# Performance work log

Hardware: AMD Instinct MI355X
Metric: run time of the kernel (lower is better)

Reference implementation:

```python
import jax, jax.numpy as jnp
import numpy as np

N = 50000      # nodes
E = 800000     # edges (avg degree 16)
H = 128        # hidden_nf
NORM_FACTOR = 100.0   # normalization_factor, aggregation 'sum'
NORM_CONST = 1.0      # norm_constant (effective_constant = max(1, 1.0))
EPS = 1e-8


def silu(v):
    return v * jax.nn.sigmoid(v)


def setup_inputs() -> dict:
    key = jax.random.key(0)
    ks = jax.random.split(key, 16)
    IN_E = 2 * H + 2  # edge MLP input: h[row] | h[col] | [radial, edge_attr]

    def w(k, shape, scale=0.05):
        return jax.random.normal(k, shape, dtype=jnp.float32) * scale

    return {
        "h": jax.random.normal(ks[0], (N, H), dtype=jnp.float32),
        "x": jax.random.normal(ks[1], (N, 3), dtype=jnp.float32),
        "edge_index": jax.random.randint(ks[2], (2, E), 0, N, dtype=jnp.int32),
        "edge_attr": jax.random.normal(ks[3], (E, 1), dtype=jnp.float32),
        "node_mask": jnp.ones((N, 1), dtype=jnp.float32),
        "edge_mask": jnp.ones((E, 1), dtype=jnp.float32),
        # 2 stacked GCL layers (identical shapes -> stacked on leading dim)
        "gcl_e_w1": w(ks[4], (2, IN_E, H)), "gcl_e_b1": jnp.zeros((2, H), jnp.float32),
        "gcl_e_w2": w(ks[5], (2, H, H)),    "gcl_e_b2": jnp.zeros((2, H), jnp.float32),
        "gcl_a_w":  w(ks[6], (2, H, 1)),    "gcl_a_b":  jnp.zeros((2, 1), jnp.float32),
        "gcl_n_w1": w(ks[7], (2, 2 * H, H)),"gcl_n_b1": jnp.zeros((2, H), jnp.float32),
        "gcl_n_w2": w(ks[8], (2, H, H)),    "gcl_n_b2": jnp.zeros((2, H), jnp.float32),
        # EquivariantUpdate coord MLP (last layer xavier gain 0.001 -> tiny, no bias)
        "c_w1": w(ks[9], (IN_E, H)), "c_b1": jnp.zeros((H,), jnp.float32),
        "c_w2": w(ks[10], (H, H)),   "c_b2": jnp.zeros((H,), jnp.float32),
        "c_w3": w(ks[11], (H, 1), 0.001),
    }


def reference(h, x, edge_index, edge_attr, node_mask, edge_mask,
              gcl_e_w1, gcl_e_b1, gcl_e_w2, gcl_e_b2, gcl_a_w, gcl_a_b,
              gcl_n_w1, gcl_n_b1, gcl_n_w2, gcl_n_b2,
              c_w1, c_b1, c_w2, c_b2, c_w3):
    row, col = edge_index[0], edge_index[1]
    n_nodes = h.shape[0]

    # coord2diff
    diff = x[row] - x[col]                                  # [E,3]
    radial = jnp.sum(diff * diff, axis=1, keepdims=True)    # [E,1]
    norm = jnp.sqrt(radial + EPS)
    coord_diff = diff / (norm + NORM_CONST)

    # edge_attr = cat([distances, edge_attr])  -> edge_feat_nf = 2
    ea = jnp.concatenate([radial, edge_attr], axis=1)       # [E,2]

    # n_layers=2 GCLs with attention
    for i in range(2):
        einp = jnp.concatenate([h[row], h[col], ea], axis=1)             # [E,258]
        mij = silu(silu(einp @ gcl_e_w1[i] + gcl_e_b1[i]) @ gcl_e_w2[i] + gcl_e_b2[i])
        att = jax.nn.sigmoid(mij @ gcl_a_w[i] + gcl_a_b[i])
        ef = mij * att * edge_mask                                       # [E,H]
        agg = jax.ops.segment_sum(ef, row, num_segments=n_nodes) / NORM_FACTOR
        ninp = jnp.concatenate([h, agg], axis=1)                         # [N,2H]
        h = h + (silu(ninp @ gcl_n_w1[i] + gcl_n_b1[i]) @ gcl_n_w2[i] + gcl_n_b2[i])
        h = h * node_mask

    # EquivariantUpdate (tanh=False, reflection_equiv=True -> no cross term)
    einp = jnp.concatenate([h[row], h[col], ea], axis=1)
    phi = silu(silu(einp @ c_w1 + c_b1) @ c_w2 + c_b2) @ c_w3            # [E,1]
    trans = coord_diff * phi * edge_mask                                 # [E,3]
    aggx = jax.ops.segment_sum(trans, row, num_segments=n_nodes) / NORM_FACTOR
    x = (x + aggx) * node_mask

    h = h * node_mask
    return (h, x)
```

## Files before the change

### kernel.cpp

```cpp
#include <hip/hip_runtime.h>
#include <hip/hip_bf16.h>
#include <math.h>
#include <string.h>

#define DEV __device__ __forceinline__

typedef __bf16 bf16;
typedef bf16 bf16x8 __attribute__((ext_vector_type(8)));
typedef bf16 bf16x2 __attribute__((ext_vector_type(2)));
typedef float f32x4 __attribute__((ext_vector_type(4)));
typedef unsigned int uint;

constexpr int N_NODES = 50000;
constexpr int N_EDGES = 800000;
constexpr int H = 128;
constexpr int NB_SCAN = (N_NODES + 255) / 256;

DEV float fsilu(float x) { return x / (1.f + __expf(-x)); }
DEV float fsigmoid(float x) { return 1.f / (1.f + __expf(-x)); }


__global__ void transpose_pad_kernel(bf16* __restrict__ dst, const float* __restrict__ src,
                                     int K, int Nf, int KP) {
    int idx = blockIdx.x * 256 + threadIdx.x;
    if (idx >= Nf * KP) return;
    int n = idx / KP, k = idx - n * KP;
    dst[idx] = (k < K) ? (bf16)src[k * Nf + n] : (bf16)0.f;
}

__global__ void h_init_kernel(const float* __restrict__ h, float* __restrict__ h_cur,
                              bf16* __restrict__ h_bf, int n) {
    int i = blockIdx.x * 256 + threadIdx.x;
    if (i < n) { float v = h[i]; h_cur[i] = v; h_bf[i] = (bf16)v; }
}

__global__ void out_h_kernel(const float* __restrict__ h_cur, const float* __restrict__ nmask,
                             float* __restrict__ out) {
    int i = blockIdx.x * 256 + threadIdx.x;
    if (i < N_NODES * H) out[i] = h_cur[i] * nmask[i >> 7];
}


__global__ void count_kernel(const int* __restrict__ ei, int* __restrict__ deg) {
    int e = blockIdx.x * 256 + threadIdx.x;
    if (e < N_EDGES) atomicAdd(&deg[ei[e]], 1);
}

__global__ void scan1_kernel(const int* __restrict__ deg, int* __restrict__ off,
                             int* __restrict__ bsum) {
    __shared__ int s[256];
    int t = threadIdx.x, i = blockIdx.x * 256 + t;
    int v = (i < N_NODES) ? deg[i] : 0;
    s[t] = v;
    __syncthreads();
#pragma unroll
    for (int st = 1; st < 256; st <<= 1) {
        int x = (t >= st) ? s[t - st] : 0;
        __syncthreads();
        s[t] += x;
        __syncthreads();
    }
    if (i < N_NODES) off[i] = s[t] - v;
    if (t == 255) bsum[blockIdx.x] = s[255];
}

__global__ void scan2_kernel(int* __restrict__ bsum) {
    __shared__ int s[256];
    int t = threadIdx.x;
    int v = (t < NB_SCAN) ? bsum[t] : 0;
    s[t] = v;
    __syncthreads();
#pragma unroll
    for (int st = 1; st < 256; st <<= 1) {
        int x = (t >= st) ? s[t - st] : 0;
        __syncthreads();
        s[t] += x;
        __syncthreads();
    }
    if (t < NB_SCAN) bsum[t] = s[t] - v;
}

__global__ void scan3_kernel(int* __restrict__ off, int* __restrict__ cursor,
                             const int* __restrict__ bsum) {
    int i = blockIdx.x * 256 + threadIdx.x;
    if (i >= N_NODES) return;
    int o = off[i] + bsum[blockIdx.x];
    off[i] = o;
    cursor[i] = o;
}

__global__ void fill2_kernel(const int* __restrict__ ei, const float* __restrict__ x,
                             const float* __restrict__ eattr, const float* __restrict__ emask,
                             int* __restrict__ cursor, uint* __restrict__ rc_pm,
                             bf16* __restrict__ ea_pm, bf16* __restrict__ em_pm) {
    int e = blockIdx.x * 256 + threadIdx.x;
    if (e >= N_EDGES) return;
    int r = ei[e], c = ei[N_EDGES + e];
    int slot = atomicAdd(&cursor[r], 1);
    rc_pm[slot] = ((uint)r << 16) | (uint)c;
    float dx = x[r * 3 + 0] - x[c * 3 + 0];
    float dy = x[r * 3 + 1] - x[c * 3 + 1];
    float dz = x[r * 3 + 2] - x[c * 3 + 2];
    float radial = dx * dx + dy * dy + dz * dz;
    ea_pm[(size_t)slot * 2 + 0] = (bf16)radial;
    ea_pm[(size_t)slot * 2 + 1] = (bf16)eattr[e];
    em_pm[slot] = (bf16)emask[e];
}


__global__ __launch_bounds__(256) void gather_h_kernel(
    const bf16* __restrict__ ef, const int* __restrict__ off, const int* __restrict__ deg,
    bf16* __restrict__ agg_bf) {
    int t = threadIdx.x, lane = t & 63, wv = t >> 6;
    int n = blockIdx.x * 4 + wv;
    if (n >= N_NODES) return;
    int st = off[n], dg = deg[n];
    const bf16* bp = ef + (size_t)st * H + lane * 2;
    float s0 = 0.f, s1 = 0.f;
    for (int k = 0; k < dg; ++k) {
        uint v = *(const uint*)(bp + (size_t)k * H);
        s0 += __uint_as_float(v << 16);
        s1 += __uint_as_float(v & 0xffff0000u);
    }
    bf16x2 o;
    o[0] = (bf16)(s0 * 0.01f);
    o[1] = (bf16)(s1 * 0.01f);
    *(bf16x2*)(agg_bf + (size_t)n * H + lane * 2) = o;
}

__global__ __launch_bounds__(256) void gather_x_kernel(
    const float* __restrict__ trans, const int* __restrict__ off, const int* __restrict__ deg,
    const float* __restrict__ x, const float* __restrict__ nmask, float* __restrict__ outx) {
    int t = threadIdx.x, lane = t & 63, wv = t >> 6;
    int n = blockIdx.x * 4 + wv;
    if (n >= N_NODES) return;
    int st = off[n], dg = deg[n];
    float sx = 0.f, sy = 0.f, sz = 0.f;
    for (int k = lane; k < dg; k += 64) {
        const float* tp = trans + (size_t)(st + k) * 3;
        sx += tp[0];
        sy += tp[1];
        sz += tp[2];
    }
#pragma unroll
    for (int m = 1; m < 64; m <<= 1) {
        sx += __shfl_xor(sx, m);
        sy += __shfl_xor(sy, m);
        sz += __shfl_xor(sz, m);
    }
    if (lane == 0) {
        float nm = nmask[n];
        outx[n * 3 + 0] = (x[n * 3 + 0] + sx * 0.01f) * nm;
        outx[n * 3 + 1] = (x[n * 3 + 1] + sy * 0.01f) * nm;
        outx[n * 3 + 2] = (x[n * 3 + 2] + sz * 0.01f) * nm;
    }
}


template <int KCHUNKS, int ASTRIDE, int BSTRIDE>
DEV void wave_gemm(const bf16* A_lds, const bf16* __restrict__ Bt,
                   f32x4 (&acc)[4][2], int lr, int lg, int wv) {
#pragma unroll
    for (int kk = 0; kk < KCHUNKS; ++kk) {
        int ko = kk * 32 + lg * 8;
        bf16x8 a[4], b[2];
#pragma unroll
        for (int er = 0; er < 4; ++er)
            a[er] = *(const bf16x8*)(A_lds + (er * 16 + lr) * ASTRIDE + ko);
#pragma unroll
        for (int j = 0; j < 2; ++j)
            b[j] = *(const bf16x8*)(Bt + (size_t)((wv * 2 + j) * 16 + lr) * BSTRIDE + ko);
#pragma unroll
        for (int er = 0; er < 4; ++er)
#pragma unroll
            for (int j = 0; j < 2; ++j)
                acc[er][j] = __builtin_amdgcn_mfma_f32_16x16x32_bf16(a[er], b[j], acc[er][j], 0, 0, 0);
    }
}

DEV void epi_silu_store(const f32x4 (&acc)[4][2], const float* __restrict__ bias,
                        bf16* out_lds, int OSTRIDE, int lr, int lg, int wv) {
    float b0 = bias[(wv * 2 + 0) * 16 + lr];
    float b1 = bias[(wv * 2 + 1) * 16 + lr];
#pragma unroll
    for (int er = 0; er < 4; ++er) {
#pragma unroll
        for (int j = 0; j < 2; ++j) {
            float bb = j ? b1 : b0;
            int fcol = (wv * 2 + j) * 16 + lr;
#pragma unroll
            for (int r = 0; r < 4; ++r) {
                int rrow = er * 16 + lg * 4 + r;
                out_lds[rrow * OSTRIDE + fcol] = (bf16)fsilu(acc[er][j][r] + bb);
            }
        }
    }
}

DEV void epi_silu_store_swz(const f32x4 (&acc)[4][2], const float* __restrict__ bias,
                            bf16* out_lds, int lr, int lg, int wv) {
    float b0 = bias[(wv * 2 + 0) * 16 + lr];
    float b1 = bias[(wv * 2 + 1) * 16 + lr];
#pragma unroll
    for (int er = 0; er < 4; ++er) {
#pragma unroll
        for (int j = 0; j < 2; ++j) {
            float bb = j ? b1 : b0;
            int fcol = (wv * 2 + j) * 16 + lr;
#pragma unroll
            for (int r = 0; r < 4; ++r) {
                int rrow = er * 16 + lg * 4 + r;
                int sl = (fcol >> 3) ^ (rrow & 7);
                out_lds[rrow * 128 + sl * 8 + (fcol & 7)] = (bf16)fsilu(acc[er][j][r] + bb);
            }
        }
    }
}

template <int MODE>
__global__ __launch_bounds__(256, 4) void edge_kernel(
    const bf16* __restrict__ h_bf, const bf16* __restrict__ ea_pm,
    const uint* __restrict__ rc_pm, const bf16* __restrict__ em_pm,
    const bf16* __restrict__ w1t, const float* __restrict__ b1,
    const bf16* __restrict__ w2t, const float* __restrict__ b2,
    const float* __restrict__ avec, const float* __restrict__ abias,
    const float* __restrict__ xg, bf16* __restrict__ efout, float* __restrict__ trans) {
    __shared__ __align__(16) bf16 AR[64 * 128];
    __shared__ __align__(16) bf16 AC[64 * 128];
    __shared__ __align__(16) float avec_l[128];
    __shared__ int row_l[64];
    __shared__ int col_l[64];
    __shared__ float em_l[64];

    int t = threadIdx.x, lane = t & 63, wv = t >> 6;
    int lr = lane & 15, lg = lane >> 4;
    int ebase = blockIdx.x * 64;

    {
        int rsub = lane >> 4;
        int slot = lane & 15;
#pragma unroll
        for (int u = 0; u < 4; ++u) {
            int r = wv * 16 + u * 4 + rsub;
            uint rc = rc_pm[ebase + r];
            int nr = (int)(rc >> 16);
            int nc = (int)(rc & 0xffffu);
            int sl = slot ^ (r & 7);
            const bf16* gpr = h_bf + (size_t)nr * H + sl * 8;
            __builtin_amdgcn_global_load_lds(
                (const __attribute__((address_space(1))) void*)gpr,
                (__attribute__((address_space(3))) void*)&AR[(wv * 16 + u * 4) * 128],
                16, 0, 0);
            const bf16* gpc = h_bf + (size_t)nc * H + sl * 8;
            __builtin_amdgcn_global_load_lds(
                (const __attribute__((address_space(1))) void*)gpc,
                (__attribute__((address_space(3))) void*)&AC[(wv * 16 + u * 4) * 128],
                16, 0, 0);
        }
    }
    if (t < 64) {
        uint rc = rc_pm[ebase + t];
        row_l[t] = (int)(rc >> 16);
        col_l[t] = (int)(rc & 0xffffu);
        em_l[t] = (float)em_pm[ebase + t];
    } else if (t < 192) {
        avec_l[t - 64] = avec[t - 64];
    }

    uint eau[4];
#pragma unroll
    for (int er = 0; er < 4; ++er)
        eau[er] = *(const uint*)(ea_pm + (size_t)(ebase + er * 16 + lr) * 2);

    const bf16* bp0 = w1t + (size_t)((wv * 2 + 0) * 16 + lr) * 288 + lg * 8;
    const bf16* bp1 = w1t + (size_t)((wv * 2 + 1) * 16 + lr) * 288 + lg * 8;

    uint4 bv0[5], bv1[5];
#pragma unroll
    for (int kk = 0; kk < 5; ++kk) {
        bv0[kk] = *(const uint4*)(bp0 + kk * 32);
        bv1[kk] = *(const uint4*)(bp1 + kk * 32);
    }
#pragma unroll
    for (int kk = 0; kk < 5; ++kk) {
        asm volatile("" ::"v"(bv0[kk].x), "v"(bv0[kk].y), "v"(bv0[kk].z), "v"(bv0[kk].w));
        asm volatile("" ::"v"(bv1[kk].x), "v"(bv1[kk].y), "v"(bv1[kk].z), "v"(bv1[kk].w));
    }

    __syncthreads();

    f32x4 acc[4][2];
#pragma unroll
    for (int er = 0; er < 4; ++er)
#pragma unroll
        for (int j = 0; j < 2; ++j) acc[er][j] = (f32x4)0.f;

#pragma unroll
    for (int kk = 0; kk < 8; ++kk) {
        const bf16* Ab = (kk < 4) ? AR : AC;
        int k4 = kk & 3;
        bf16x8 a[4], b[2];
        b[0] = (kk < 5) ? __builtin_bit_cast(bf16x8, bv0[kk]) : *(const bf16x8*)(bp0 + kk * 32);
        b[1] = (kk < 5) ? __builtin_bit_cast(bf16x8, bv1[kk]) : *(const bf16x8*)(bp1 + kk * 32);
#pragma unroll
        for (int er = 0; er < 4; ++er) {
            int sl = (k4 * 4 + lg) ^ (lr & 7);
            a[er] = *(const bf16x8*)(Ab + (er * 16 + lr) * 128 + sl * 8);
        }
#pragma unroll
        for (int er = 0; er < 4; ++er)
#pragma unroll
            for (int j = 0; j < 2; ++j)
                acc[er][j] = __builtin_amdgcn_mfma_f32_16x16x32_bf16(a[er], b[j], acc[er][j], 0, 0, 0);
    }
    {
        bf16x8 a[4], b[2];
        b[0] = *(const bf16x8*)(bp0 + 8 * 32);
        b[1] = *(const bf16x8*)(bp1 + 8 * 32);
#pragma unroll
        for (int er = 0; er < 4; ++er) {
            bf16x8 f = (bf16x8)(bf16)0.f;
            if (lg == 0) {
                bf16x2 ep;
                memcpy(&ep, &eau[er], 4);
                f[0] = ep[0];
                f[1] = ep[1];
            }
            a[er] = f;
        }
#pragma unroll
        for (int er = 0; er < 4; ++er)
#pragma unroll
            for (int j = 0; j < 2; ++j)
                acc[er][j] = __builtin_amdgcn_mfma_f32_16x16x32_bf16(a[er], b[j], acc[er][j], 0, 0, 0);
    }
    __syncthreads();

    epi_silu_store_swz(acc, b1, AR, lr, lg, wv);
    __syncthreads();

    f32x4 acc2[4][2];
#pragma unroll
    for (int er = 0; er < 4; ++er)
#pragma unroll
        for (int j = 0; j < 2; ++j) acc2[er][j] = (f32x4)0.f;
    {
        const bf16* cp0 = w2t + (size_t)((wv * 2 + 0) * 16 + lr) * 128 + lg * 8;
        const bf16* cp1 = w2t + (size_t)((wv * 2 + 1) * 16 + lr) * 128 + lg * 8;
#pragma unroll
        for (int kk = 0; kk < 4; ++kk) {
            bf16x8 a[4], b[2];
            b[0] = *(const bf16x8*)(cp0 + kk * 32);
            b[1] = *(const bf16x8*)(cp1 + kk * 32);
#pragma unroll
            for (int er = 0; er < 4; ++er) {
                int sl = (kk * 4 + lg) ^ (lr & 7);
                a[er] = *(const bf16x8*)(AR + (er * 16 + lr) * 128 + sl * 8);
            }
#pragma unroll
            for (int er = 0; er < 4; ++er)
#pragma unroll
                for (int j = 0; j < 2; ++j)
                    acc2[er][j] = __builtin_amdgcn_mfma_f32_16x16x32_bf16(a[er], b[j], acc2[er][j], 0, 0, 0);
        }
    }

    bf16* mij = AC;
    epi_silu_store_swz(acc2, b2, mij, lr, lg, wv);
    __syncthreads();

    int el = t >> 2, q = t & 3;
    float part = 0.f;
    bf16x8 mv[4];
#pragma unroll
    for (int c = 0; c < 4; ++c) {
        int sl = (q * 4 + c) ^ (el & 7);
        mv[c] = *(const bf16x8*)(mij + el * 128 + sl * 8);
        f32x4 av0 = *(const f32x4*)(avec_l + q * 32 + c * 8);
        f32x4 av1 = *(const f32x4*)(avec_l + q * 32 + c * 8 + 4);
#pragma unroll
        for (int jj = 0; jj < 4; ++jj) part += (float)mv[c][jj] * av0[jj];
#pragma unroll
        for (int jj = 0; jj < 4; ++jj) part += (float)mv[c][4 + jj] * av1[jj];
    }
    part += __shfl_xor(part, 1);
    part += __shfl_xor(part, 2);

    if (MODE == 0) {
        float att = fsigmoid(part + abias[0]);
        float scale = att * em_l[el];
        bf16* edst = efout + (size_t)(ebase + el) * H + q * 32;
#pragma unroll
        for (int c = 0; c < 4; ++c) {
            bf16x8 o;
#pragma unroll
            for (int jj = 0; jj < 8; ++jj) o[jj] = (bf16)((float)mv[c][jj] * scale);
            *(bf16x8*)(edst + c * 8) = o;
        }
    } else {
        if (q == 0) {
            int rr = row_l[el], cc = col_l[el];
            float dx = xg[rr * 3 + 0] - xg[cc * 3 + 0];
            float dy = xg[rr * 3 + 1] - xg[cc * 3 + 1];
            float dz = xg[rr * 3 + 2] - xg[cc * 3 + 2];
            float radial = dx * dx + dy * dy + dz * dz;
            float inv = 1.f / (sqrtf(radial + 1e-8f) + 1.f);
            float s = part * em_l[el] * inv;
            int sI = ebase + el;
            trans[sI * 3 + 0] = dx * s;
            trans[sI * 3 + 1] = dy * s;
            trans[sI * 3 + 2] = dz * s;
        }
    }
}

__global__ __launch_bounds__(256, 2) void node_kernel(
    float* __restrict__ h_cur, bf16* __restrict__ h_bf, const bf16* __restrict__ agg_bf,
    const bf16* __restrict__ w1t, const float* __restrict__ b1,
    const bf16* __restrict__ w2t, const float* __restrict__ b2,
    const float* __restrict__ nmask) {
    constexpr int SRN = 264;
    constexpr int TRN = 136;
    __shared__ __align__(16) bf16 ninp[64 * SRN];
    __shared__ __align__(16) bf16 t1[64 * TRN];

    int t = threadIdx.x, lane = t & 63, wv = t >> 6;
    int lr = lane & 15, lg = lane >> 4;
    int nbase = blockIdx.x * 64;

    {
        int nl = t >> 2, q = t & 3;
        int node = nbase + nl;
        bf16* dst = ninp + nl * SRN;
        if (node < N_NODES) {
            const float4* hr = (const float4*)(h_cur + (size_t)node * H);
            const bf16* ar = agg_bf + (size_t)node * H;
#pragma unroll
            for (int pp = 0; pp < 8; ++pp) {
                int ch = pp * 4 + q;
                float4 v = hr[ch];
                dst[ch * 4 + 0] = (bf16)v.x; dst[ch * 4 + 1] = (bf16)v.y;
                dst[ch * 4 + 2] = (bf16)v.z; dst[ch * 4 + 3] = (bf16)v.w;
            }
#pragma unroll
            for (int pp = 0; pp < 4; ++pp) {
                int ch = pp * 4 + q;
                *(bf16x8*)(dst + 128 + ch * 8) = *(const bf16x8*)(ar + ch * 8);
            }
        } else {
#pragma unroll
            for (int pp = 0; pp < 8; ++pp) {
                int ch = pp * 4 + q;
#pragma unroll
                for (int k = 0; k < 4; ++k) {
                    dst[ch * 4 + k] = (bf16)0.f;
                    dst[128 + ch * 4 + k] = (bf16)0.f;
                }
            }
        }
    }
    __syncthreads();

    f32x4 acc[4][2];
#pragma unroll
    for (int er = 0; er < 4; ++er)
#pragma unroll
        for (int j = 0; j < 2; ++j) acc[er][j] = (f32x4)0.f;
    wave_gemm<8, SRN, 256>(ninp, w1t, acc, lr, lg, wv);
    epi_silu_store(acc, b1, t1, TRN, lr, lg, wv);
    __syncthreads();

    f32x4 acc2[4][2];
#pragma unroll
    for (int er = 0; er < 4; ++er)
#pragma unroll
        for (int j = 0; j < 2; ++j) acc2[er][j] = (f32x4)0.f;
    wave_gemm<4, TRN, 128>(t1, w2t, acc2, lr, lg, wv);

    float bb0 = b2[(wv * 2 + 0) * 16 + lr];
    float bb1 = b2[(wv * 2 + 1) * 16 + lr];
#pragma unroll
    for (int er = 0; er < 4; ++er) {
#pragma unroll
        for (int j = 0; j < 2; ++j) {
            float bb = j ? bb1 : bb0;
            int feat = (wv * 2 + j) * 16 + lr;
#pragma unroll
            for (int r = 0; r < 4; ++r) {
                int node = nbase + er * 16 + lg * 4 + r;
                if (node < N_NODES) {
                    size_t idx = (size_t)node * H + feat;
                    float nm = nmask[node];
                    float v = (h_cur[idx] + acc2[er][j][r] + bb) * nm;
                    h_cur[idx] = v;
                    h_bf[idx] = (bf16)v;
                }
            }
        }
    }
}

extern "C" void kernel_launch(void* const* d_in, const int* in_sizes, int n_in,
                              void* d_out, int out_size, void* d_ws, size_t ws_size,
                              hipStream_t stream) {
    (void)in_sizes; (void)n_in; (void)out_size; (void)ws_size;
    const float* h_in  = (const float*)d_in[0];
    const float* x_in  = (const float*)d_in[1];
    const int*   ei    = (const int*)d_in[2];
    const float* eattr = (const float*)d_in[3];
    const float* nmask = (const float*)d_in[4];
    const float* emask = (const float*)d_in[5];
    const float* e_w1  = (const float*)d_in[6];
    const float* e_b1  = (const float*)d_in[7];
    const float* e_w2  = (const float*)d_in[8];
    const float* e_b2  = (const float*)d_in[9];
    const float* a_w   = (const float*)d_in[10];
    const float* a_b   = (const float*)d_in[11];
    const float* n_w1  = (const float*)d_in[12];
    const float* n_b1  = (const float*)d_in[13];
    const float* n_w2  = (const float*)d_in[14];
    const float* n_b2  = (const float*)d_in[15];
    const float* c_w1  = (const float*)d_in[16];
    const float* c_b1  = (const float*)d_in[17];
    const float* c_w2  = (const float*)d_in[18];
    const float* c_b2  = (const float*)d_in[19];
    const float* c_w3  = (const float*)d_in[20];
    float* out = (float*)d_out;

    char* p = (char*)d_ws;
    auto alloc = [&](size_t bytes) { char* r = p; p += (bytes + 255) & ~(size_t)255; return r; };
    float* h_cur  = (float*)alloc((size_t)N_NODES * H * 4);
    bf16*  h_bf   = (bf16*) alloc((size_t)N_NODES * H * 2);
    bf16*  agg_bf = (bf16*) alloc((size_t)N_NODES * H * 2);
    bf16*  ea_pm  = (bf16*) alloc((size_t)N_EDGES * 2 * 2);
    bf16*  ef     = (bf16*) alloc((size_t)N_EDGES * H * 2);
    float* trans  = (float*)ef;
    int*   deg    = (int*)  alloc((size_t)N_NODES * 4);
    int*   off    = (int*)  alloc((size_t)N_NODES * 4);
    int*   cursor = (int*)  alloc((size_t)N_NODES * 4);
    int*   bsum   = (int*)  alloc((size_t)NB_SCAN * 4);
    uint*  rc_pm  = (uint*) alloc((size_t)N_EDGES * 4);
    bf16*  em_pm  = (bf16*) alloc((size_t)N_EDGES * 2);
    bf16*  e_w1t  = (bf16*) alloc((size_t)2 * 128 * 288 * 2);
    bf16*  e_w2t  = (bf16*) alloc((size_t)2 * 128 * 128 * 2);
    bf16*  n_w1t  = (bf16*) alloc((size_t)2 * 128 * 256 * 2);
    bf16*  n_w2t  = (bf16*) alloc((size_t)2 * 128 * 128 * 2);
    bf16*  c_w1t  = (bf16*) alloc((size_t)128 * 288 * 2);
    bf16*  c_w2t  = (bf16*) alloc((size_t)128 * 128 * 2);

    auto tp = [&](bf16* dst, const float* src, int K, int KP) {
        int tot = 128 * KP;
        transpose_pad_kernel<<<(tot + 255) / 256, 256, 0, stream>>>(dst, src, K, 128, KP);
    };
    tp(e_w1t, e_w1, 258, 288);               tp(e_w1t + 128 * 288, e_w1 + 258 * 128, 258, 288);
    tp(e_w2t, e_w2, 128, 128);               tp(e_w2t + 128 * 128, e_w2 + 128 * 128, 128, 128);
    tp(n_w1t, n_w1, 256, 256);               tp(n_w1t + 128 * 256, n_w1 + 256 * 128, 256, 256);
    tp(n_w2t, n_w2, 128, 128);               tp(n_w2t + 128 * 128, n_w2 + 128 * 128, 128, 128);
    tp(c_w1t, c_w1, 258, 288);
    tp(c_w2t, c_w2, 128, 128);

    h_init_kernel<<<(N_NODES * H + 255) / 256, 256, 0, stream>>>(h_in, h_cur, h_bf, N_NODES * H);

    hipMemsetAsync(deg, 0, (size_t)N_NODES * 4, stream);
    count_kernel<<<(N_EDGES + 255) / 256, 256, 0, stream>>>(ei, deg);
    scan1_kernel<<<NB_SCAN, 256, 0, stream>>>(deg, off, bsum);
    scan2_kernel<<<1, 256, 0, stream>>>(bsum);
    scan3_kernel<<<NB_SCAN, 256, 0, stream>>>(off, cursor, bsum);
    fill2_kernel<<<(N_EDGES + 255) / 256, 256, 0, stream>>>(
        ei, x_in, eattr, emask, cursor, rc_pm, ea_pm, em_pm);

    int ngrid = (N_NODES + 3) / 4;
    for (int i = 0; i < 2; ++i) {
        edge_kernel<0><<<N_EDGES / 64, 256, 0, stream>>>(
            h_bf, ea_pm, rc_pm, em_pm,
            e_w1t + (size_t)i * 128 * 288, e_b1 + i * H,
            e_w2t + (size_t)i * 128 * 128, e_b2 + i * H,
            a_w + i * H, a_b + i, nullptr, ef, nullptr);
        gather_h_kernel<<<ngrid, 256, 0, stream>>>(ef, off, deg, agg_bf);
        node_kernel<<<(N_NODES + 63) / 64, 256, 0, stream>>>(
            h_cur, h_bf, agg_bf,
            n_w1t + (size_t)i * 128 * 256, n_b1 + i * H,
            n_w2t + (size_t)i * 128 * 128, n_b2 + i * H, nmask);
    }
    edge_kernel<1><<<N_EDGES / 64, 256, 0, stream>>>(
        h_bf, ea_pm, rc_pm, em_pm,
        c_w1t, c_b1, c_w2t, c_b2, c_w3, nullptr, x_in, nullptr, trans);
    gather_x_kernel<<<ngrid, 256, 0, stream>>>(trans, off, deg, x_in, nmask,
                                               out + (size_t)N_NODES * H);

    out_h_kernel<<<(N_NODES * H + 255) / 256, 256, 0, stream>>>(h_cur, nmask, out);
}
```

Measured before the change: 906.6 us.

## Split first edge-MLP layer into per-node projections P and Q gathered per edge

The first edge-MLP layer is factored algebraically: h[row]·W_r and h[col]·W_c are computed once per node in a new pq_kernel (P with bias, Q without), and each edge then sums P[row]+Q[col] plus rank-1 radial and edge_attr terms before SiLU. This removes the per-edge K=258 GEMM, leaving only the second 128x128 GEMM in the edge kernel, which shrinks LDS use and raises the occupancy bound. The fill kernel no longer computes radial (the edge kernel recomputes it from x), and the cursor array is dropped by reusing off, with degree derived from adjacent offsets. The cost is an extra node-level GEMM per layer and two bf16 row gathers per edge, plus an extra bf16 rounding of P and Q.

```diff
diff --git a/kernel.cpp b/kernel.cpp
--- a/kernel.cpp
+++ b/kernel.cpp
@@ -28,10 +28,9 @@
     dst[idx] = (k < K) ? (bf16)src[k * Nf + n] : (bf16)0.f;
 }
 
-__global__ void h_init_kernel(const float* __restrict__ h, float* __restrict__ h_cur,
-                              bf16* __restrict__ h_bf, int n) {
+__global__ void h_init_kernel(const float* __restrict__ h, float* __restrict__ h_cur, int n) {
     int i = blockIdx.x * 256 + threadIdx.x;
-    if (i < n) { float v = h[i]; h_cur[i] = v; h_bf[i] = (bf16)v; }
+    if (i < n) h_cur[i] = h[i];
 }
 
 __global__ void out_h_kernel(const float* __restrict__ h_cur, const float* __restrict__ nmask,
@@ -80,41 +79,114 @@
     if (t < NB_SCAN) bsum[t] = s[t] - v;
 }
 
-__global__ void scan3_kernel(int* __restrict__ off, int* __restrict__ cursor,
-                             const int* __restrict__ bsum) {
+__global__ void scan3_kernel(int* __restrict__ off, const int* __restrict__ bsum) {
     int i = blockIdx.x * 256 + threadIdx.x;
     if (i >= N_NODES) return;
-    int o = off[i] + bsum[blockIdx.x];
-    off[i] = o;
-    cursor[i] = o;
-}
-
-__global__ void fill2_kernel(const int* __restrict__ ei, const float* __restrict__ x,
-                             const float* __restrict__ eattr, const float* __restrict__ emask,
-                             int* __restrict__ cursor, uint* __restrict__ rc_pm,
-                             bf16* __restrict__ ea_pm, bf16* __restrict__ em_pm) {
+    off[i] += bsum[blockIdx.x];
+}
+
+__global__ void fill2_kernel(const int* __restrict__ ei, const float* __restrict__ eattr,
+                             const float* __restrict__ emask, int* __restrict__ off,
+                             uint* __restrict__ rc_pm, bf16* __restrict__ eaem_pm) {
     int e = blockIdx.x * 256 + threadIdx.x;
     if (e >= N_EDGES) return;
     int r = ei[e], c = ei[N_EDGES + e];
-    int slot = atomicAdd(&cursor[r], 1);
+    int slot = atomicAdd(&off[r], 1);
     rc_pm[slot] = ((uint)r << 16) | (uint)c;
-    float dx = x[r * 3 + 0] - x[c * 3 + 0];
-    float dy = x[r * 3 + 1] - x[c * 3 + 1];
-    float dz = x[r * 3 + 2] - x[c * 3 + 2];
-    float radial = dx * dx + dy * dy + dz * dz;
-    ea_pm[(size_t)slot * 2 + 0] = (bf16)radial;
-    ea_pm[(size_t)slot * 2 + 1] = (bf16)eattr[e];
-    em_pm[slot] = (bf16)emask[e];
+    eaem_pm[(size_t)slot * 2 + 0] = (bf16)eattr[e];
+    eaem_pm[(size_t)slot * 2 + 1] = (bf16)emask[e];
+}
+
+__global__ __launch_bounds__(256, 2) void pq_kernel(
+    const float* __restrict__ h_cur, const bf16* __restrict__ w1t,
+    const float* __restrict__ b1, bf16* __restrict__ P, bf16* __restrict__ Q) {
+    __shared__ __align__(16) bf16 hs[64 * 128];
+    int t = threadIdx.x, lane = t & 63, wv = t >> 6;
+    int lr = lane & 15, lg = lane >> 4;
+    int nbase = blockIdx.x * 64;
+
+    {
+        int nl = t >> 2, q = t & 3;
+        int node = nbase + nl;
+        if (node < N_NODES) {
+            const float4* hr = (const float4*)(h_cur + (size_t)node * H);
+#pragma unroll
+            for (int c = 0; c < 4; ++c) {
+                float4 v0 = hr[q * 8 + c * 2];
+                float4 v1 = hr[q * 8 + c * 2 + 1];
+                bf16x8 o;
+                o[0] = (bf16)v0.x; o[1] = (bf16)v0.y; o[2] = (bf16)v0.z; o[3] = (bf16)v0.w;
+                o[4] = (bf16)v1.x; o[5] = (bf16)v1.y; o[6] = (bf16)v1.z; o[7] = (bf16)v1.w;
+                int sl = (q * 4 + c) ^ (nl & 7);
+                *(bf16x8*)(hs + nl * 128 + sl * 8) = o;
+            }
+        } else {
+#pragma unroll
+            for (int c = 0; c < 4; ++c) {
+                int sl = (q * 4 + c) ^ (nl & 7);
+                *(bf16x8*)(hs + nl * 128 + sl * 8) = (bf16x8)(bf16)0.f;
+            }
+        }
+    }
+    __syncthreads();
+
+    f32x4 aP[4][2], aQ[4][2];
+#pragma unroll
+    for (int er = 0; er < 4; ++er)
+#pragma unroll
+        for (int j = 0; j < 2; ++j) { aP[er][j] = (f32x4)0.f; aQ[er][j] = (f32x4)0.f; }
+
+    const bf16* bp0 = w1t + (size_t)((wv * 2 + 0) * 16 + lr) * 256 + lg * 8;
+    const bf16* bp1 = w1t + (size_t)((wv * 2 + 1) * 16 + lr) * 256 + lg * 8;
+#pragma unroll
+    for (int kk = 0; kk < 4; ++kk) {
+        bf16x8 a[4];
+#pragma unroll
+        for (int er = 0; er < 4; ++er) {
+            int sl = (kk * 4 + lg) ^ (lr & 7);
+            a[er] = *(const bf16x8*)(hs + (er * 16 + lr) * 128 + sl * 8);
+        }
+        bf16x8 bP0 = *(const bf16x8*)(bp0 + kk * 32);
+        bf16x8 bP1 = *(const bf16x8*)(bp1 + kk * 32);
+        bf16x8 bQ0 = *(const bf16x8*)(bp0 + 128 + kk * 32);
+        bf16x8 bQ1 = *(const bf16x8*)(bp1 + 128 + kk * 32);
+#pragma unroll
+        for (int er = 0; er < 4; ++er) {
+            aP[er][0] = __builtin_amdgcn_mfma_f32_16x16x32_bf16(a[er], bP0, aP[er][0], 0, 0, 0);
+            aP[er][1] = __builtin_amdgcn_mfma_f32_16x16x32_bf16(a[er], bP1, aP[er][1], 0, 0, 0);
+            aQ[er][0] = __builtin_amdgcn_mfma_f32_16x16x32_bf16(a[er], bQ0, aQ[er][0], 0, 0, 0);
+            aQ[er][1] = __builtin_amdgcn_mfma_f32_16x16x32_bf16(a[er], bQ1, aQ[er][1], 0, 0, 0);
+        }
+    }
+
+    float bb0 = b1[(wv * 2 + 0) * 16 + lr];
+    float bb1v = b1[(wv * 2 + 1) * 16 + lr];
+#pragma unroll
+    for (int er = 0; er < 4; ++er) {
+#pragma unroll
+        for (int j = 0; j < 2; ++j) {
+            int feat = (wv * 2 + j) * 16 + lr;
+            float bb = j ? bb1v : bb0;
+#pragma unroll
+            for (int r = 0; r < 4; ++r) {
+                int node = nbase + er * 16 + lg * 4 + r;
+                if (node < N_NODES) {
+                    P[(size_t)node * H + feat] = (bf16)(aP[er][j][r] + bb);
+                    Q[(size_t)node * H + feat] = (bf16)(aQ[er][j][r]);
+                }
+            }
+        }
+    }
 }
 
 
 __global__ __launch_bounds__(256) void gather_h_kernel(
-    const bf16* __restrict__ ef, const int* __restrict__ off, const int* __restrict__ deg,
-    bf16* __restrict__ agg_bf) {
+    const bf16* __restrict__ ef, const int* __restrict__ off, bf16* __restrict__ agg_bf) {
     int t = threadIdx.x, lane = t & 63, wv = t >> 6;
     int n = blockIdx.x * 4 + wv;
     if (n >= N_NODES) return;
-    int st = off[n], dg = deg[n];
+    int st = (n == 0) ? 0 : off[n - 1];
+    int dg = off[n] - st;
     const bf16* bp = ef + (size_t)st * H + lane * 2;
     float s0 = 0.f, s1 = 0.f;
     for (int k = 0; k < dg; ++k) {
@@ -129,12 +201,13 @@
 }
 
 __global__ __launch_bounds__(256) void gather_x_kernel(
-    const float* __restrict__ trans, const int* __restrict__ off, const int* __restrict__ deg,
+    const float* __restrict__ trans, const int* __restrict__ off,
     const float* __restrict__ x, const float* __restrict__ nmask, float* __restrict__ outx) {
     int t = threadIdx.x, lane = t & 63, wv = t >> 6;
     int n = blockIdx.x * 4 + wv;
     if (n >= N_NODES) return;
-    int st = off[n], dg = deg[n];
+    int st = (n == 0) ? 0 : off[n - 1];
+    int dg = off[n] - st;
     float sx = 0.f, sy = 0.f, sz = 0.f;
     for (int k = lane; k < dg; k += 64) {
         const float* tp = trans + (size_t)(st + k) * 3;
@@ -218,125 +291,56 @@
 }
 
 template <int MODE>
-__global__ __launch_bounds__(256, 4) void edge_kernel(
-    const bf16* __restrict__ h_bf, const bf16* __restrict__ ea_pm,
-    const uint* __restrict__ rc_pm, const bf16* __restrict__ em_pm,
-    const bf16* __restrict__ w1t, const float* __restrict__ b1,
+__global__ __launch_bounds__(256, 6) void edge_kernel(
+    const bf16* __restrict__ P, const bf16* __restrict__ Q,
+    const uint* __restrict__ rc_pm, const bf16* __restrict__ eaem_pm,
+    const float* __restrict__ xg,
+    const float* __restrict__ w_r, const float* __restrict__ w_e,
     const bf16* __restrict__ w2t, const float* __restrict__ b2,
     const float* __restrict__ avec, const float* __restrict__ abias,
-    const float* __restrict__ xg, bf16* __restrict__ efout, float* __restrict__ trans) {
-    __shared__ __align__(16) bf16 AR[64 * 128];
-    __shared__ __align__(16) bf16 AC[64 * 128];
-    __shared__ __align__(16) float avec_l[128];
-    __shared__ int row_l[64];
-    __shared__ int col_l[64];
-    __shared__ float em_l[64];
+    bf16* __restrict__ efout, float* __restrict__ trans) {
+    __shared__ __align__(16) bf16 T[64 * 128];
 
     int t = threadIdx.x, lane = t & 63, wv = t >> 6;
     int lr = lane & 15, lg = lane >> 4;
     int ebase = blockIdx.x * 64;
-
-    {
-        int rsub = lane >> 4;
-        int slot = lane & 15;
-#pragma unroll
-        for (int u = 0; u < 4; ++u) {
-            int r = wv * 16 + u * 4 + rsub;
-            uint rc = rc_pm[ebase + r];
-            int nr = (int)(rc >> 16);
-            int nc = (int)(rc & 0xffffu);
-            int sl = slot ^ (r & 7);
-            const bf16* gpr = h_bf + (size_t)nr * H + sl * 8;
-            __builtin_amdgcn_global_load_lds(
-                (const __attribute__((address_space(1))) void*)gpr,
-                (__attribute__((address_space(3))) void*)&AR[(wv * 16 + u * 4) * 128],
-                16, 0, 0);
-            const bf16* gpc = h_bf + (size_t)nc * H + sl * 8;
-            __builtin_amdgcn_global_load_lds(
-                (const __attribute__((address_space(1))) void*)gpc,
-                (__attribute__((address_space(3))) void*)&AC[(wv * 16 + u * 4) * 128],
-                16, 0, 0);
-        }
-    }
-    if (t < 64) {
-        uint rc = rc_pm[ebase + t];
-        row_l[t] = (int)(rc >> 16);
-        col_l[t] = (int)(rc & 0xffffu);
-        em_l[t] = (float)em_pm[ebase + t];
-    } else if (t < 192) {
-        avec_l[t - 64] = avec[t - 64];
-    }
-
-    uint eau[4];
-#pragma unroll
-    for (int er = 0; er < 4; ++er)
-        eau[er] = *(const uint*)(ea_pm + (size_t)(ebase + er * 16 + lr) * 2);
-
-    const bf16* bp0 = w1t + (size_t)((wv * 2 + 0) * 16 + lr) * 288 + lg * 8;
-    const bf16* bp1 = w1t + (size_t)((wv * 2 + 1) * 16 + lr) * 288 + lg * 8;
-
-    uint4 bv0[5], bv1[5];
-#pragma unroll
-    for (int kk = 0; kk < 5; ++kk) {
-        bv0[kk] = *(const uint4*)(bp0 + kk * 32);
-        bv1[kk] = *(const uint4*)(bp1 + kk * 32);
-    }
-#pragma unroll
-    for (int kk = 0; kk < 5; ++kk) {
-        asm volatile("" ::"v"(bv0[kk].x), "v"(bv0[kk].y), "v"(bv0[kk].z), "v"(bv0[kk].w));
-        asm volatile("" ::"v"(bv1[kk].x), "v"(bv1[kk].y), "v"(bv1[kk].z), "v"(bv1[kk].w));
-    }
-
-    __syncthreads();
-
-    f32x4 acc[4][2];
-#pragma unroll
-    for (int er = 0; er < 4; ++er)
-#pragma unroll
-        for (int j = 0; j < 2; ++j) acc[er][j] = (f32x4)0.f;
-
-#pragma unroll
-    for (int kk = 0; kk < 8; ++kk) {
-        const bf16* Ab = (kk < 4) ? AR : AC;
-        int k4 = kk & 3;
-        bf16x8 a[4], b[2];
-        b[0] = (kk < 5) ? __builtin_bit_cast(bf16x8, bv0[kk]) : *(const bf16x8*)(bp0 + kk * 32);
-        b[1] = (kk < 5) ? __builtin_bit_cast(bf16x8, bv1[kk]) : *(const bf16x8*)(bp1 + kk * 32);
-#pragma unroll
-        for (int er = 0; er < 4; ++er) {
-            int sl = (k4 * 4 + lg) ^ (lr & 7);
-            a[er] = *(const bf16x8*)(Ab + (er * 16 + lr) * 128 + sl * 8);
-        }
-#pragma unroll
-        for (int er = 0; er < 4; ++er)
-#pragma unroll
-            for (int j = 0; j < 2; ++j)
-                acc[er][j] = __builtin_amdgcn_mfma_f32_16x16x32_bf16(a[er], b[j], acc[er][j], 0, 0, 0);
-    }
-    {
-        bf16x8 a[4], b[2];
-        b[0] = *(const bf16x8*)(bp0 + 8 * 32);
-        b[1] = *(const bf16x8*)(bp1 + 8 * 32);
-#pragma unroll
-        for (int er = 0; er < 4; ++er) {
-            bf16x8 f = (bf16x8)(bf16)0.f;
-            if (lg == 0) {
-                bf16x2 ep;
-                memcpy(&ep, &eau[er], 4);
-                f[0] = ep[0];
-                f[1] = ep[1];
-            }
-            a[er] = f;
-        }
-#pragma unroll
-        for (int er = 0; er < 4; ++er)
-#pragma unroll
-            for (int j = 0; j < 2; ++j)
-                acc[er][j] = __builtin_amdgcn_mfma_f32_16x16x32_bf16(a[er], b[j], acc[er][j], 0, 0, 0);
-    }
-    __syncthreads();
-
-    epi_silu_store_swz(acc, b1, AR, lr, lg, wv);
+    int el = t >> 2, q = t & 3;
+
+    uint rc = rc_pm[ebase + el];
+    int rr = (int)(rc >> 16), cc = (int)(rc & 0xffffu);
+    float dx = xg[rr * 3 + 0] - xg[cc * 3 + 0];
+    float dy = xg[rr * 3 + 1] - xg[cc * 3 + 1];
+    float dz = xg[rr * 3 + 2] - xg[cc * 3 + 2];
+    float radial = dx * dx + dy * dy + dz * dz;
+    uint eu = *(const uint*)(eaem_pm + (size_t)(ebase + el) * 2);
+    bf16x2 ep = __builtin_bit_cast(bf16x2, eu);
+    float eattr = (float)ep[0];
+    float em = (float)ep[1];
+
+    const bf16* Pp = P + (size_t)rr * H + q * 32;
+    const bf16* Qp = Q + (size_t)cc * H + q * 32;
+#pragma unroll
+    for (int c = 0; c < 4; ++c) {
+        bf16x8 pv = *(const bf16x8*)(Pp + c * 8);
+        bf16x8 qv = *(const bf16x8*)(Qp + c * 8);
+        f32x4 wr0 = *(const f32x4*)(w_r + q * 32 + c * 8);
+        f32x4 wr1 = *(const f32x4*)(w_r + q * 32 + c * 8 + 4);
+        f32x4 we0 = *(const f32x4*)(w_e + q * 32 + c * 8);
+        f32x4 we1 = *(const f32x4*)(w_e + q * 32 + c * 8 + 4);
+        bf16x8 o;
+#pragma unroll
+        for (int jj = 0; jj < 4; ++jj) {
+            float v = (float)pv[jj] + (float)qv[jj] + radial * wr0[jj] + eattr * we0[jj];
+            o[jj] = (bf16)fsilu(v);
+        }
+#pragma unroll
+        for (int jj = 0; jj < 4; ++jj) {
+            float v = (float)pv[4 + jj] + (float)qv[4 + jj] + radial * wr1[jj] + eattr * we1[jj];
+            o[4 + jj] = (bf16)fsilu(v);
+        }
+        int sl = (q * 4 + c) ^ (el & 7);
+        *(bf16x8*)(T + el * 128 + sl * 8) = o;
+    }
     __syncthreads();
 
     f32x4 acc2[4][2];
@@ -355,7 +359,7 @@
 #pragma unroll
             for (int er = 0; er < 4; ++er) {
                 int sl = (kk * 4 + lg) ^ (lr & 7);
-                a[er] = *(const bf16x8*)(AR + (er * 16 + lr) * 128 + sl * 8);
+                a[er] = *(const bf16x8*)(T + (er * 16 + lr) * 128 + sl * 8);
             }
 #pragma unroll
             for (int er = 0; er < 4; ++er)
@@ -364,20 +368,19 @@
                     acc2[er][j] = __builtin_amdgcn_mfma_f32_16x16x32_bf16(a[er], b[j], acc2[er][j], 0, 0, 0);
         }
     }
-
-    bf16* mij = AC;
-    epi_silu_store_swz(acc2, b2, mij, lr, lg, wv);
-    __syncthreads();
-
-    int el = t >> 2, q = t & 3;
+    __syncthreads();
+
+    epi_silu_store_swz(acc2, b2, T, lr, lg, wv);
+    __syncthreads();
+
     float part = 0.f;
     bf16x8 mv[4];
 #pragma unroll
     for (int c = 0; c < 4; ++c) {
         int sl = (q * 4 + c) ^ (el & 7);
-        mv[c] = *(const bf16x8*)(mij + el * 128 + sl * 8);
-        f32x4 av0 = *(const f32x4*)(avec_l + q * 32 + c * 8);
-        f32x4 av1 = *(const f32x4*)(avec_l + q * 32 + c * 8 + 4);
+        mv[c] = *(const bf16x8*)(T + el * 128 + sl * 8);
+        f32x4 av0 = *(const f32x4*)(avec + q * 32 + c * 8);
+        f32x4 av1 = *(const f32x4*)(avec + q * 32 + c * 8 + 4);
 #pragma unroll
         for (int jj = 0; jj < 4; ++jj) part += (float)mv[c][jj] * av0[jj];
 #pragma unroll
@@ -388,7 +391,7 @@
 
     if (MODE == 0) {
         float att = fsigmoid(part + abias[0]);
-        float scale = att * em_l[el];
+        float scale = att * em;
         bf16* edst = efout + (size_t)(ebase + el) * H + q * 32;
 #pragma unroll
         for (int c = 0; c < 4; ++c) {
@@ -399,13 +402,8 @@
         }
     } else {
         if (q == 0) {
-            int rr = row_l[el], cc = col_l[el];
-            float dx = xg[rr * 3 + 0] - xg[cc * 3 + 0];
-            float dy = xg[rr * 3 + 1] - xg[cc * 3 + 1];
-            float dz = xg[rr * 3 + 2] - xg[cc * 3 + 2];
-            float radial = dx * dx + dy * dy + dz * dz;
             float inv = 1.f / (sqrtf(radial + 1e-8f) + 1.f);
-            float s = part * em_l[el] * inv;
+            float s = part * em * inv;
             int sI = ebase + el;
             trans[sI * 3 + 0] = dx * s;
             trans[sI * 3 + 1] = dy * s;
@@ -415,7 +413,7 @@
 }
 
 __global__ __launch_bounds__(256, 2) void node_kernel(
-    float* __restrict__ h_cur, bf16* __restrict__ h_bf, const bf16* __restrict__ agg_bf,
+    float* __restrict__ h_cur, const bf16* __restrict__ agg_bf,
     const bf16* __restrict__ w1t, const float* __restrict__ b1,
     const bf16* __restrict__ w2t, const float* __restrict__ b2,
     const float* __restrict__ nmask) {
@@ -491,9 +489,7 @@
                 if (node < N_NODES) {
                     size_t idx = (size_t)node * H + feat;
                     float nm = nmask[node];
-                    float v = (h_cur[idx] + acc2[er][j][r] + bb) * nm;
-                    h_cur[idx] = v;
-                    h_bf[idx] = (bf16)v;
+                    h_cur[idx] = (h_cur[idx] + acc2[er][j][r] + bb) * nm;
                 }
             }
         }
@@ -530,62 +526,67 @@
     char* p = (char*)d_ws;
     auto alloc = [&](size_t bytes) { char* r = p; p += (bytes + 255) & ~(size_t)255; return r; };
     float* h_cur  = (float*)alloc((size_t)N_NODES * H * 4);
-    bf16*  h_bf   = (bf16*) alloc((size_t)N_NODES * H * 2);
-    bf16*  agg_bf = (bf16*) alloc((size_t)N_NODES * H * 2);
-    bf16*  ea_pm  = (bf16*) alloc((size_t)N_EDGES * 2 * 2);
+    bf16*  Pb     = (bf16*) alloc((size_t)N_NODES * H * 2);
+    bf16*  Qb     = (bf16*) alloc((size_t)N_NODES * H * 2);
+    bf16*  agg_bf = Qb;
     bf16*  ef     = (bf16*) alloc((size_t)N_EDGES * H * 2);
     float* trans  = (float*)ef;
     int*   deg    = (int*)  alloc((size_t)N_NODES * 4);
     int*   off    = (int*)  alloc((size_t)N_NODES * 4);
-    int*   cursor = (int*)  alloc((size_t)N_NODES * 4);
     int*   bsum   = (int*)  alloc((size_t)NB_SCAN * 4);
     uint*  rc_pm  = (uint*) alloc((size_t)N_EDGES * 4);
-    bf16*  em_pm  = (bf16*) alloc((size_t)N_EDGES * 2);
-    bf16*  e_w1t  = (bf16*) alloc((size_t)2 * 128 * 288 * 2);
+    bf16*  eaem_pm= (bf16*) alloc((size_t)N_EDGES * 2 * 2);
+    bf16*  e_w1t  = (bf16*) alloc((size_t)2 * 128 * 256 * 2);
     bf16*  e_w2t  = (bf16*) alloc((size_t)2 * 128 * 128 * 2);
     bf16*  n_w1t  = (bf16*) alloc((size_t)2 * 128 * 256 * 2);
     bf16*  n_w2t  = (bf16*) alloc((size_t)2 * 128 * 128 * 2);
-    bf16*  c_w1t  = (bf16*) alloc((size_t)128 * 288 * 2);
+    bf16*  c_w1t  = (bf16*) alloc((size_t)128 * 256 * 2);
     bf16*  c_w2t  = (bf16*) alloc((size_t)128 * 128 * 2);
 
     auto tp = [&](bf16* dst, const float* src, int K, int KP) {
         int tot = 128 * KP;
         transpose_pad_kernel<<<(tot + 255) / 256, 256, 0, stream>>>(dst, src, K, 128, KP);
     };
-    tp(e_w1t, e_w1, 258, 288);               tp(e_w1t + 128 * 288, e_w1 + 258 * 128, 258, 288);
+    tp(e_w1t, e_w1, 258, 256);               tp(e_w1t + 128 * 256, e_w1 + 258 * 128, 258, 256);
     tp(e_w2t, e_w2, 128, 128);               tp(e_w2t + 128 * 128, e_w2 + 128 * 128, 128, 128);
     tp(n_w1t, n_w1, 256, 256);               tp(n_w1t + 128 * 256, n_w1 + 256 * 128, 256, 256);
     tp(n_w2t, n_w2, 128, 128);               tp(n_w2t + 128 * 128, n_w2 + 128 * 128, 128, 128);
-    tp(c_w1t, c_w1, 258, 288);
+    tp(c_w1t, c_w1, 258, 256);
     tp(c_w2t, c_w2, 128, 128);
 
-    h_init_kernel<<<(N_NODES * H + 255) / 256, 256, 0, stream>>>(h_in, h_cur, h_bf, N_NODES * H);
+    h_init_kernel<<<(N_NODES * H + 255) / 256, 256, 0, stream>>>(h_in, h_cur, N_NODES * H);
 
     hipMemsetAsync(deg, 0, (size_t)N_NODES * 4, stream);
     count_kernel<<<(N_EDGES + 255) / 256, 256, 0, stream>>>(ei, deg);
     scan1_kernel<<<NB_SCAN, 256, 0, stream>>>(deg, off, bsum);
     scan2_kernel<<<1, 256, 0, stream>>>(bsum);
-    scan3_kernel<<<NB_SCAN, 256, 0, stream>>>(off, cursor, bsum);
+    scan3_kernel<<<NB_SCAN, 256, 0, stream>>>(off, bsum);
     fill2_kernel<<<(N_EDGES + 255) / 256, 256, 0, stream>>>(
-        ei, x_in, eattr, emask, cursor, rc_pm, ea_pm, em_pm);
+        ei, eattr, emask, off, rc_pm, eaem_pm);
 
     int ngrid = (N_NODES + 3) / 4;
+    int pqgrid = (N_NODES + 63) / 64;
     for (int i = 0; i < 2; ++i) {
+        pq_kernel<<<pqgrid, 256, 0, stream>>>(
+            h_cur, e_w1t + (size_t)i * 128 * 256, e_b1 + i * H, Pb, Qb);
         edge_kernel<0><<<N_EDGES / 64, 256, 0, stream>>>(
-            h_bf, ea_pm, rc_pm, em_pm,
-            e_w1t + (size_t)i * 128 * 288, e_b1 + i * H,
+            Pb, Qb, rc_pm, eaem_pm, x_in,
+            e_w1 + (size_t)i * 258 * 128 + 256 * 128,
+            e_w1 + (size_t)i * 258 * 128 + 257 * 128,
             e_w2t + (size_t)i * 128 * 128, e_b2 + i * H,
-            a_w + i * H, a_b + i, nullptr, ef, nullptr);
-        gather_h_kernel<<<ngrid, 256, 0, stream>>>(ef, off, deg, agg_bf);
+            a_w + i * H, a_b + i, ef, nullptr);
+        gather_h_kernel<<<ngrid, 256, 0, stream>>>(ef, off, agg_bf);
         node_kernel<<<(N_NODES + 63) / 64, 256, 0, stream>>>(
-            h_cur, h_bf, agg_bf,
+            h_cur, agg_bf,
             n_w1t + (size_t)i * 128 * 256, n_b1 + i * H,
             n_w2t + (size_t)i * 128 * 128, n_b2 + i * H, nmask);
     }
+    pq_kernel<<<pqgrid, 256, 0, stream>>>(h_cur, c_w1t, c_b1, Pb, Qb);
     edge_kernel<1><<<N_EDGES / 64, 256, 0, stream>>>(
-        h_bf, ea_pm, rc_pm, em_pm,
-        c_w1t, c_b1, c_w2t, c_b2, c_w3, nullptr, x_in, nullptr, trans);
-    gather_x_kernel<<<ngrid, 256, 0, stream>>>(trans, off, deg, x_in, nmask,
+        Pb, Qb, rc_pm, eaem_pm, x_in,
+        c_w1 + 256 * 128, c_w1 + 257 * 128,
+        c_w2t, c_b2, c_w3, nullptr, nullptr, trans);
+    gather_x_kernel<<<ngrid, 256, 0, stream>>>(trans, off, x_in, nmask,
                                                out + (size_t)N_NODES * H);
 
     out_h_kernel<<<(N_NODES * H + 255) / 256, 256, 0, stream>>>(h_cur, nmask, out);
```

Measured after the change: 1.057 ms. +16.6%, slower.
